# Kernel tuning notes

Measured on AMD Instinct MI355X. Metric: run time of the kernel, lower is better.

The kernel has to match this reference:

```python
import jax, jax.numpy as jnp
import numpy as np

B, L, D_IN, D_EDGE, H, D = 2, 384, 256, 128, 8, 32
SCALE = D ** (-0.5)


def setup_inputs() -> dict:
    key = jax.random.key(0)
    ks = jax.random.split(key, 12)
    hd = H * D
    s_in = D_IN ** -0.5
    s_e = D_EDGE ** -0.5
    return {
        "node_feat": jax.random.normal(ks[0], (B, L, D_IN), jnp.float32),
        "edge_feat": jax.random.normal(ks[1], (B, L, L, D_EDGE), jnp.float32),
        "edge_mask": (jax.random.uniform(ks[2], (B, L, L)) > 0.15).astype(jnp.float32),
        "Wq": jax.random.normal(ks[3], (D_IN, hd), jnp.float32) * s_in,
        "bq": jnp.zeros((hd,), jnp.float32),
        "Wk": jax.random.normal(ks[4], (D_IN, hd), jnp.float32) * s_in,
        "bk": jnp.zeros((hd,), jnp.float32),
        "Wv": jax.random.normal(ks[5], (D_IN, hd), jnp.float32) * s_in,
        "bv": jnp.zeros((hd,), jnp.float32),
        "We": jax.random.normal(ks[6], (D_EDGE, hd), jnp.float32) * s_e,
        "Wu": jax.random.normal(ks[7], (D_IN, hd), jnp.float32) * s_in,
        "bu": jnp.zeros((hd,), jnp.float32),
    }


def _split_heads(t):
    # (b, l, h*d) -> (b, h, l, d)
    b, l, _ = t.shape
    return t.reshape(b, l, H, D).transpose(0, 2, 1, 3)


def reference(node_feat, edge_feat, edge_mask, Wq, bq, Wk, bk, Wv, bv, We, Wu, bu):
    q = _split_heads(node_feat @ Wq + bq)
    k = _split_heads(node_feat @ Wk + bk)
    v = _split_heads(node_feat @ Wv + bv)
    # edge embedding: (b, i, j, h*d) -> (b, h, i, j, d)
    b, l = edge_feat.shape[0], edge_feat.shape[1]
    e = (edge_feat @ We).reshape(b, l, l, H, D).transpose(0, 3, 1, 2, 4)
    logit = jnp.einsum('bhid,bhjd->bhij', q, k)
    logit = logit + jnp.einsum('bhid,bhijd->bhij', q, e)
    att = logit * SCALE
    att = att + ((1.0 - edge_mask) * -1e9)[:, None, :, :]
    att = jax.nn.softmax(att, axis=-1)  # dropout is identity in eval / p=0
    updated = jnp.einsum('bhij,bhjd->bhid', att, v)
    updated = updated + jnp.einsum('bhij,bhijd->bhid', att, e)
    updated = updated.transpose(0, 2, 1, 3).reshape(b, l, H * D)
    return (node_feat @ Wu + bu) + updated
```

## Files before the change

kernel.cpp:

```cpp
#include <hip/hip_runtime.h>
#include <hip/hip_bf16.h>
#include <cstdint>

#define NB 2
#define LL 384
#define DIN 256
#define DE 128
#define NH 8
#define DH 32
#define HD 256
#define TJ 32
#define NTILES (LL / TJ)
#define SCALE 0.17677669529663687f

typedef __attribute__((ext_vector_type(8))) short bf16x8;
typedef __attribute__((ext_vector_type(4))) float f32x4;

static __device__ __forceinline__ unsigned short f2bf(float f) {
    uint32_t u = __builtin_bit_cast(uint32_t, f);
    u += 0x7FFF + ((u >> 16) & 1);
    return (unsigned short)(u >> 16);
}
static __device__ __forceinline__ float bf2f(unsigned short u) {
    return __builtin_bit_cast(float, (uint32_t)u << 16);
}
static __device__ __forceinline__ float getf4(const float4& v, int k) {
    return k == 0 ? v.x : k == 1 ? v.y : k == 2 ? v.z : v.w;
}

__global__ __launch_bounds__(128) void prep_we(const float* __restrict__ We,
                                               unsigned short* __restrict__ WeT) {
    const int n = blockIdx.x;
    const int k = threadIdx.x;
    WeT[n * DE + k] = f2bf(We[(size_t)k * HD + n]);
}

__global__ __launch_bounds__(256) void proj_kernel(
    const float* __restrict__ node,
    const float* __restrict__ Wq, const float* __restrict__ bq,
    const float* __restrict__ Wk, const float* __restrict__ bk,
    const float* __restrict__ Wv, const float* __restrict__ bv,
    const float* __restrict__ Wu, const float* __restrict__ bu,
    unsigned short* __restrict__ qb16, unsigned short* __restrict__ kb16,
    float* __restrict__ vb, float* __restrict__ ub)
{
    __shared__ __align__(16) float rows[4][DIN];
    const int t  = threadIdx.x;
    const int r0 = blockIdx.x * 4;

    #pragma unroll
    for (int r = 0; r < 4; ++r)
        rows[r][t] = node[(size_t)(r0 + r) * DIN + t];
    __syncthreads();

    float aq[4], ak[4], av[4], au[4];
    {
        const float vq = bq[t], vk = bk[t], vv = bv[t], vu = bu[t];
        #pragma unroll
        for (int r = 0; r < 4; ++r) { aq[r] = vq; ak[r] = vk; av[r] = vv; au[r] = vu; }
    }

    for (int f4 = 0; f4 < DIN / 4; ++f4) {
        float4 xv[4];
        #pragma unroll
        for (int r = 0; r < 4; ++r)
            xv[r] = *(const float4*)&rows[r][f4 * 4];
        #pragma unroll
        for (int k = 0; k < 4; ++k) {
            const int f = f4 * 4 + k;
            const float wq = Wq[(size_t)f * HD + t];
            const float wk = Wk[(size_t)f * HD + t];
            const float wv = Wv[(size_t)f * HD + t];
            const float wu = Wu[(size_t)f * HD + t];
            #pragma unroll
            for (int r = 0; r < 4; ++r) {
                const float x = getf4(xv[r], k);
                aq[r] += x * wq; ak[r] += x * wk; av[r] += x * wv; au[r] += x * wu;
            }
        }
    }

    #pragma unroll
    for (int r = 0; r < 4; ++r) {
        const size_t o = (size_t)(r0 + r) * HD + t;
        qb16[o] = f2bf(aq[r]); kb16[o] = f2bf(ak[r]);
        vb[o] = av[r]; ub[o] = au[r];
    }
}

__global__ __launch_bounds__(256) void vt_kernel(const float* __restrict__ vb,
                                                 unsigned short* __restrict__ vT) {
    __shared__ float tile[64][65];
    int blk = blockIdx.x;
    const int b  = blk / 24; blk %= 24;
    const int jt = blk / 4;
    const int ct = blk % 4;
    const int j0 = jt * 64, c0 = ct * 64;
    const int t  = threadIdx.x;
    const int c  = t & 63, j4 = t >> 6;
    #pragma unroll
    for (int rr = 0; rr < 16; ++rr) {
        const int j = j4 + 4 * rr;
        tile[j][c] = vb[(size_t)(b * LL + j0 + j) * HD + c0 + c];
    }
    __syncthreads();
    const int jj = t & 63, c4 = t >> 6;
    #pragma unroll
    for (int rr = 0; rr < 16; ++rr) {
        const int cc = c4 + 4 * rr;
        vT[(size_t)(b * HD + c0 + cc) * LL + j0 + jj] = f2bf(tile[jj][cc]);
    }
}

__global__ __launch_bounds__(256) void qk_kernel(
    const unsigned short* __restrict__ qb16, const unsigned short* __restrict__ kb16,
    const float* __restrict__ mask, float* __restrict__ logit_pre)
{
    int idx = blockIdx.x;
    const int jt = idx % 6; idx /= 6;
    const int it = idx % 6; idx /= 6;
    const int h  = idx % NH;
    const int b  = idx / NH;
    const int t    = threadIdx.x;
    const int lane = t & 63;
    const int w    = t >> 6;
    const int lid  = lane & 15;
    const int g    = lane >> 4;
    const int i0 = it * 64 + w * 16;
    const int j0 = jt * 64;

    const bf16x8 afr = *(const bf16x8*)&qb16[(size_t)(b * LL + i0 + lid) * HD + h * DH + g * 8];
    f32x4 acc[4];
    #pragma unroll
    for (int jj = 0; jj < 4; ++jj) {
        const bf16x8 bfrg = *(const bf16x8*)&kb16[(size_t)(b * LL + j0 + jj * 16 + lid) * HD + h * DH + g * 8];
        acc[jj] = __builtin_amdgcn_mfma_f32_16x16x32_bf16(afr, bfrg, (f32x4){0.f,0.f,0.f,0.f}, 0, 0, 0);
    }
    #pragma unroll
    for (int jj = 0; jj < 4; ++jj) {
        #pragma unroll
        for (int r = 0; r < 4; ++r) {
            const int i = i0 + 4 * g + r;
            const int j = j0 + jj * 16 + lid;
            const float lg = SCALE * acc[jj][r]
                           + (1.0f - mask[(size_t)(b * LL + i) * LL + j]) * -1e9f;
            logit_pre[((size_t)(b * NH + h) * LL + i) * LL + j] = lg;
        }
    }
}

__global__ __launch_bounds__(512, 4) void attn_kernel(
    const float* __restrict__ edge,
    const unsigned short* __restrict__ WeT,
    const float* __restrict__ logit_pre,
    const unsigned short* __restrict__ qb16,
    const unsigned short* __restrict__ vT,
    const float* __restrict__ ub,
    float* __restrict__ out)
{
    const int t    = threadIdx.x;
    const int lane = t & 63;
    const int w    = t >> 6;
    const int lid  = lane & 15;
    const int g    = lane >> 4;
    const int wb   = w * DH;
    const int bi   = blockIdx.x;
    const int b    = bi / LL;
    const int ii   = bi % LL;

    __shared__ __align__(16) unsigned short Es[2][TJ * DE];

    const float* efbase = edge + (size_t)bi * LL * DE;
    const float* lpre   = logit_pre + ((size_t)(b * NH + w) * LL + ii) * LL;
    const unsigned short* vTb = vT + (size_t)b * HD * LL;

    bf16x8 bfr[2][4];
    #pragma unroll
    for (int ct = 0; ct < 2; ++ct)
        #pragma unroll
        for (int kt = 0; kt < 4; ++kt)
            bfr[ct][kt] = *(const bf16x8*)&WeT[(size_t)(wb + ct * 16 + lid) * DE + kt * 32 + g * 8];

    float qf[2];
    #pragma unroll
    for (int ct = 0; ct < 2; ++ct)
        qf[ct] = bf2f(qb16[(size_t)bi * HD + wb + ct * 16 + lid]) * SCALE;

    const int sr = t >> 4;
    const int ci = t & 15;
    const int wchunk = (ci ^ (sr & 15)) << 3;

    const int jl_self = (((lid >> 2) & 1) << 4) + 4 * g + (lid & 3);

    float m_run = -3e38f, l_run = 0.0f;
    float out_p[2] = {0.f, 0.f};

    {
        const float* src = efbase + (size_t)sr * DE + ci * 8;
        const float4 x0 = ((const float4*)src)[0];
        const float4 x1 = ((const float4*)src)[1];
        bf16x8 p0;
        p0[0]=(short)f2bf(x0.x); p0[1]=(short)f2bf(x0.y); p0[2]=(short)f2bf(x0.z); p0[3]=(short)f2bf(x0.w);
        p0[4]=(short)f2bf(x1.x); p0[5]=(short)f2bf(x1.y); p0[6]=(short)f2bf(x1.z); p0[7]=(short)f2bf(x1.w);
        *(bf16x8*)&Es[0][sr * DE + wchunk] = p0;
    }

    for (int tile = 0; tile < NTILES; ++tile) {
        const int j0  = tile * TJ;
        const int cur = tile & 1;
        const unsigned short* Ecur = Es[cur];
        __syncthreads();

        const bool have_next = (tile + 1 < NTILES);
        float4 nx0, nx1;
        if (have_next) {
            const float* src = efbase + (size_t)(j0 + TJ + sr) * DE + ci * 8;
            nx0 = ((const float4*)src)[0];
            nx1 = ((const float4*)src)[1];
        }
        const float qkm = lpre[j0 + jl_self];
        ushort4 vld[2][2];
        #pragma unroll
        for (int ct = 0; ct < 2; ++ct)
            #pragma unroll
            for (int mm = 0; mm < 2; ++mm)
                vld[ct][mm] = *(const ushort4*)&vTb[(size_t)(wb + ct * 16 + lid) * LL + j0 + mm * 16 + 4 * g];

        f32x4 acc[2][2];
        #pragma unroll
        for (int mm = 0; mm < 2; ++mm)
            #pragma unroll
            for (int ct = 0; ct < 2; ++ct)
                acc[mm][ct] = (f32x4){0.f, 0.f, 0.f, 0.f};

        #pragma unroll
        for (int kt = 0; kt < 4; ++kt) {
            const int ch = kt * 4 + g;
            const bf16x8 a0 = *(const bf16x8*)&Ecur[lid * DE + ((ch ^ lid) << 3)];
            const bf16x8 a1 = *(const bf16x8*)&Ecur[(16 + lid) * DE + ((ch ^ lid) << 3)];
            #pragma unroll
            for (int ct = 0; ct < 2; ++ct) {
                acc[0][ct] = __builtin_amdgcn_mfma_f32_16x16x32_bf16(a0, bfr[ct][kt], acc[0][ct], 0, 0, 0);
                acc[1][ct] = __builtin_amdgcn_mfma_f32_16x16x32_bf16(a1, bfr[ct][kt], acc[1][ct], 0, 0, 0);
            }
        }

        float plog[8];
        #pragma unroll
        for (int mm = 0; mm < 2; ++mm)
            #pragma unroll
            for (int rg = 0; rg < 4; ++rg)
                plog[mm * 4 + rg] = acc[mm][0][rg] * qf[0] + acc[mm][1][rg] * qf[1];

        #pragma unroll
        for (int i2 = 0; i2 < 8; ++i2) plog[i2] += __shfl_xor(plog[i2], 8);
        float v4[4];
        {
            const bool hi = (lane & 4) != 0;
            #pragma unroll
            for (int r = 0; r < 4; ++r) {
                const float k2 = hi ? plog[4 + r] : plog[r];
                const float s2 = hi ? plog[r] : plog[4 + r];
                v4[r] = k2 + __shfl_xor(s2, 4);
            }
        }
        float v2[2];
        {
            const bool hi = (lane & 2) != 0;
            #pragma unroll
            for (int c2 = 0; c2 < 2; ++c2) {
                const float k2 = hi ? v4[2 + c2] : v4[c2];
                const float s2 = hi ? v4[c2] : v4[2 + c2];
                v2[c2] = k2 + __shfl_xor(s2, 2);
            }
        }
        float lgv;
        {
            const bool hi = (lane & 1) != 0;
            const float k2 = hi ? v2[1] : v2[0];
            const float s2 = hi ? v2[0] : v2[1];
            lgv = k2 + __shfl_xor(s2, 1);
        }
        const float lg = lgv + qkm;

        float mt = lg;
        #pragma unroll
        for (int off = 1; off < 64; off <<= 1) mt = fmaxf(mt, __shfl_xor(mt, off));
        const float mn = fmaxf(m_run, mt);
        const float p  = __expf(lg - mn);
        float ps = p;
        #pragma unroll
        for (int off = 1; off < 64; off <<= 1) ps += __shfl_xor(ps, off);
        const float fs = __expf(m_run - mn);
        l_run = l_run * fs + ps * 0.5f;
        m_run = mn;

        float pp[8];
        #pragma unroll
        for (int mm = 0; mm < 2; ++mm)
            #pragma unroll
            for (int rg = 0; rg < 4; ++rg)
                pp[mm * 4 + rg] = __shfl(p, (lane & 48) + mm * 4 + rg);

        out_p[0] *= fs; out_p[1] *= fs;
        #pragma unroll
        for (int ct = 0; ct < 2; ++ct)
            #pragma unroll
            for (int mm = 0; mm < 2; ++mm) {
                const ushort4 vv = vld[ct][mm];
                out_p[ct] += pp[mm * 4 + 0] * (bf2f(vv.x) + acc[mm][ct][0]);
                out_p[ct] += pp[mm * 4 + 1] * (bf2f(vv.y) + acc[mm][ct][1]);
                out_p[ct] += pp[mm * 4 + 2] * (bf2f(vv.z) + acc[mm][ct][2]);
                out_p[ct] += pp[mm * 4 + 3] * (bf2f(vv.w) + acc[mm][ct][3]);
            }

        if (have_next) {
            bf16x8 p0;
            p0[0]=(short)f2bf(nx0.x); p0[1]=(short)f2bf(nx0.y); p0[2]=(short)f2bf(nx0.z); p0[3]=(short)f2bf(nx0.w);
            p0[4]=(short)f2bf(nx1.x); p0[5]=(short)f2bf(nx1.y); p0[6]=(short)f2bf(nx1.z); p0[7]=(short)f2bf(nx1.w);
            *(bf16x8*)&Es[cur ^ 1][sr * DE + wchunk] = p0;
        }
    }

    #pragma unroll
    for (int ct = 0; ct < 2; ++ct) {
        out_p[ct] += __shfl_xor(out_p[ct], 16);
        out_p[ct] += __shfl_xor(out_p[ct], 32);
    }
    if (lane < 16) {
        const float inv = 1.0f / l_run;
        #pragma unroll
        for (int ct = 0; ct < 2; ++ct) {
            const int col = wb + ct * 16 + lane;
            out[(size_t)bi * HD + col] = ub[(size_t)bi * HD + col] + out_p[ct] * inv;
        }
    }
}

extern "C" void kernel_launch(void* const* d_in, const int* in_sizes, int n_in,
                              void* d_out, int out_size, void* d_ws, size_t ws_size,
                              hipStream_t stream) {
    const float* node = (const float*)d_in[0];
    const float* edge = (const float*)d_in[1];
    const float* mask = (const float*)d_in[2];
    const float* Wq   = (const float*)d_in[3];
    const float* bq   = (const float*)d_in[4];
    const float* Wk   = (const float*)d_in[5];
    const float* bk   = (const float*)d_in[6];
    const float* Wv   = (const float*)d_in[7];
    const float* bv   = (const float*)d_in[8];
    const float* We   = (const float*)d_in[9];
    const float* Wu   = (const float*)d_in[10];
    const float* bu   = (const float*)d_in[11];
    float* out = (float*)d_out;

    const size_t rowsz = (size_t)NB * LL * HD;
    float* ws   = (float*)d_ws;
    float* vb   = ws;
    float* ubuf = vb + rowsz;
    float* lpre = ubuf + rowsz;
    unsigned short* us   = (unsigned short*)(lpre + (size_t)NB * NH * LL * LL);
    unsigned short* WeT  = us;
    unsigned short* qb16 = WeT + (size_t)HD * DE;
    unsigned short* kb16 = qb16 + rowsz;
    unsigned short* vT   = kb16 + rowsz;

    hipLaunchKernelGGL(prep_we, dim3(HD), dim3(DE), 0, stream, We, WeT);
    hipLaunchKernelGGL(proj_kernel, dim3(NB * LL / 4), dim3(256), 0, stream,
                       node, Wq, bq, Wk, bk, Wv, bv, Wu, bu, qb16, kb16, vb, ubuf);
    hipLaunchKernelGGL(vt_kernel, dim3(NB * (LL / 64) * (HD / 64)), dim3(256), 0, stream,
                       vb, vT);
    hipLaunchKernelGGL(qk_kernel, dim3(NB * NH * (LL / 64) * (LL / 64)), dim3(256), 0, stream,
                       qb16, kb16, mask, lpre);
    hipLaunchKernelGGL(attn_kernel, dim3(NB * LL), dim3(512), 0, stream,
                       edge, WeT, lpre, qb16, vT, ubuf, out);
}
```

Baseline: 101.8 us.

## Reassociate edge projection: fold q into We and apply We after att·edge

Replaces the fused flash-style attention kernel with three kernels. The first precomputes q·We^T per node so edge logits come from edge·(qWe), a 128-wide product instead of projecting each edge to 256 dims. The second computes an exact two-pass softmax in place over the stored logits. The third computes att·edge and att·V with MFMA, then multiplies the aggregated edge sum by We afterwards. This cuts the edge GEMM FLOPs, but the edge tensor is now read from HBM twice and there are extra launches and a logit-buffer round trip.

New measurement: 118.7 us. 16.6% more time.

```diff
diff --git a/kernel.cpp b/kernel.cpp
--- a/kernel.cpp
+++ b/kernel.cpp
@@ -1,5 +1,4 @@
 #include <hip/hip_runtime.h>
-#include <hip/hip_bf16.h>
 #include <cstdint>
 
 #define NB 2
@@ -9,8 +8,6 @@
 #define NH 8
 #define DH 32
 #define HD 256
-#define TJ 32
-#define NTILES (LL / TJ)
 #define SCALE 0.17677669529663687f
 
 typedef __attribute__((ext_vector_type(8))) short bf16x8;
@@ -26,6 +23,12 @@
 }
 static __device__ __forceinline__ float getf4(const float4& v, int k) {
     return k == 0 ? v.x : k == 1 ? v.y : k == 2 ? v.z : v.w;
+}
+static __device__ __forceinline__ bf16x8 pack8(const float4& a, const float4& b) {
+    bf16x8 p;
+    p[0]=(short)f2bf(a.x); p[1]=(short)f2bf(a.y); p[2]=(short)f2bf(a.z); p[3]=(short)f2bf(a.w);
+    p[4]=(short)f2bf(b.x); p[5]=(short)f2bf(b.y); p[6]=(short)f2bf(b.z); p[7]=(short)f2bf(b.w);
+    return p;
 }
 
 __global__ __launch_bounds__(128) void prep_we(const float* __restrict__ We,
@@ -149,191 +152,216 @@
     }
 }
 
-__global__ __launch_bounds__(512, 4) void attn_kernel(
+__global__ __launch_bounds__(256) void qwe_kernel(
+    const unsigned short* __restrict__ qb16, const unsigned short* __restrict__ WeT,
+    unsigned short* __restrict__ qWe)
+{
+    const int bi = blockIdx.x;
+    const int t  = threadIdx.x;
+    const int h  = t >> 5;
+    const int c0 = (t & 31) * 4;
+
+    float qv[32];
+    const unsigned short* qp = &qb16[(size_t)bi * HD + h * DH];
+    #pragma unroll
+    for (int d = 0; d < 32; ++d) qv[d] = bf2f(qp[d]);
+
+    float acc0 = 0.f, acc1 = 0.f, acc2 = 0.f, acc3 = 0.f;
+    #pragma unroll
+    for (int d = 0; d < 32; ++d) {
+        const ushort4 wt = *(const ushort4*)&WeT[(size_t)(h * DH + d) * DE + c0];
+        acc0 += qv[d] * bf2f(wt.x); acc1 += qv[d] * bf2f(wt.y);
+        acc2 += qv[d] * bf2f(wt.z); acc3 += qv[d] * bf2f(wt.w);
+    }
+    unsigned short* o = &qWe[(size_t)bi * (NH * DE) + h * DE + c0];
+    o[0] = f2bf(SCALE * acc0); o[1] = f2bf(SCALE * acc1);
+    o[2] = f2bf(SCALE * acc2); o[3] = f2bf(SCALE * acc3);
+}
+
+__global__ __launch_bounds__(512, 4) void att_kernel(
     const float* __restrict__ edge,
+    const unsigned short* __restrict__ qWe,
+    float* __restrict__ lpre)
+{
+    __shared__ float red0[64], red1[64];
+    const int t = threadIdx.x, lane = t & 63, w = t >> 6;
+    const int lid = lane & 15, g = lane >> 4;
+    const int bi = blockIdx.x, b = bi / LL, ii = bi % LL;
+    const int J  = w * 48;
+    const int hq = lid & 7;
+
+    bf16x8 bfr[4];
+    const unsigned short* qwp = &qWe[(size_t)bi * (NH * DE) + hq * DE];
+    #pragma unroll
+    for (int kt = 0; kt < 4; ++kt)
+        bfr[kt] = *(const bf16x8*)&qwp[kt * 32 + g * 8];
+
+    f32x4 acc[3];
+    #pragma unroll
+    for (int mt = 0; mt < 3; ++mt) {
+        acc[mt] = (f32x4){0.f, 0.f, 0.f, 0.f};
+        const float* ef = edge + ((size_t)bi * LL + J + mt * 16 + lid) * DE;
+        #pragma unroll
+        for (int kt = 0; kt < 4; ++kt) {
+            const float4 x0 = *(const float4*)&ef[kt * 32 + g * 8];
+            const float4 x1 = *(const float4*)&ef[kt * 32 + g * 8 + 4];
+            acc[mt] = __builtin_amdgcn_mfma_f32_16x16x32_bf16(pack8(x0, x1), bfr[kt], acc[mt], 0, 0, 0);
+        }
+    }
+
+    float lg[12];
+    float* lrow = lpre + ((size_t)(b * NH + hq) * LL + ii) * LL;
+    #pragma unroll
+    for (int mt = 0; mt < 3; ++mt)
+        #pragma unroll
+        for (int r = 0; r < 4; ++r) {
+            const int j = J + mt * 16 + g * 4 + r;
+            lg[mt * 4 + r] = (lid < 8) ? (acc[mt][r] + lrow[j]) : -3e38f;
+        }
+
+    float m = lg[0];
+    #pragma unroll
+    for (int k = 1; k < 12; ++k) m = fmaxf(m, lg[k]);
+    m = fmaxf(m, __shfl_xor(m, 16));
+    m = fmaxf(m, __shfl_xor(m, 32));
+    if (lane < 8) red0[w * 8 + lane] = m;
+    __syncthreads();
+    float M = red0[hq];
+    #pragma unroll
+    for (int k = 1; k < 8; ++k) M = fmaxf(M, red0[k * 8 + hq]);
+
+    float p[12], s = 0.f;
+    #pragma unroll
+    for (int k = 0; k < 12; ++k) { p[k] = __expf(lg[k] - M); s += p[k]; }
+    s += __shfl_xor(s, 16); s += __shfl_xor(s, 32);
+    if (lane < 8) red1[w * 8 + lane] = s;
+    __syncthreads();
+    float S = 0.f;
+    #pragma unroll
+    for (int k = 0; k < 8; ++k) S += red1[k * 8 + hq];
+    const float inv = 1.0f / S;
+
+    if (lid < 8) {
+        #pragma unroll
+        for (int mt = 0; mt < 3; ++mt)
+            #pragma unroll
+            for (int r = 0; r < 4; ++r)
+                lrow[J + mt * 16 + g * 4 + r] = p[mt * 4 + r] * inv;
+    }
+}
+
+#define TJ 64
+#define NT (LL / TJ)
+__global__ __launch_bounds__(512, 4) void pv_kernel(
+    const float* __restrict__ edge,
+    const float* __restrict__ att,
+    const unsigned short* __restrict__ vT,
     const unsigned short* __restrict__ WeT,
-    const float* __restrict__ logit_pre,
-    const unsigned short* __restrict__ qb16,
-    const unsigned short* __restrict__ vT,
     const float* __restrict__ ub,
     float* __restrict__ out)
 {
-    const int t    = threadIdx.x;
-    const int lane = t & 63;
-    const int w    = t >> 6;
-    const int lid  = lane & 15;
-    const int g    = lane >> 4;
-    const int wb   = w * DH;
-    const int bi   = blockIdx.x;
-    const int b    = bi / LL;
-    const int ii   = bi % LL;
-
     __shared__ __align__(16) unsigned short Es[2][TJ * DE];
-
+    __shared__ __align__(16) unsigned short atts[NH * LL];
+    __shared__ float smA[NH * DE];
+    __shared__ float avs[HD];
+
+    const int t = threadIdx.x, lane = t & 63, w = t >> 6;
+    const int lid = lane & 15, g = lane >> 4;
+    const int bi = blockIdx.x, b = bi / LL, ii = bi % LL;
     const float* efbase = edge + (size_t)bi * LL * DE;
-    const float* lpre   = logit_pre + ((size_t)(b * NH + w) * LL + ii) * LL;
-    const unsigned short* vTb = vT + (size_t)b * HD * LL;
-
-    bf16x8 bfr[2][4];
-    #pragma unroll
-    for (int ct = 0; ct < 2; ++ct)
-        #pragma unroll
-        for (int kt = 0; kt < 4; ++kt)
-            bfr[ct][kt] = *(const bf16x8*)&WeT[(size_t)(wb + ct * 16 + lid) * DE + kt * 32 + g * 8];
-
-    float qf[2];
-    #pragma unroll
-    for (int ct = 0; ct < 2; ++ct)
-        qf[ct] = bf2f(qb16[(size_t)bi * HD + wb + ct * 16 + lid]) * SCALE;
-
-    const int sr = t >> 4;
-    const int ci = t & 15;
-    const int wchunk = (ci ^ (sr & 15)) << 3;
-
-    const int jl_self = (((lid >> 2) & 1) << 4) + 4 * g + (lid & 3);
-
-    float m_run = -3e38f, l_run = 0.0f;
-    float out_p[2] = {0.f, 0.f};
 
     {
+        const float* ar = att + ((size_t)(b * NH + w) * LL + ii) * LL;
+        #pragma unroll
+        for (int k = 0; k < 3; ++k) {
+            const int j2 = (lane + 64 * k) * 2;
+            const float2 x = *(const float2*)&ar[j2];
+            const unsigned int pk = ((unsigned int)f2bf(x.y) << 16) | (unsigned int)f2bf(x.x);
+            *(unsigned int*)&atts[w * LL + j2] = pk;
+        }
+    }
+    #pragma unroll
+    for (int q = 0; q < 2; ++q) {
+        const int id = t + q * 512, sr = id >> 4, ci = id & 15;
         const float* src = efbase + (size_t)sr * DE + ci * 8;
-        const float4 x0 = ((const float4*)src)[0];
-        const float4 x1 = ((const float4*)src)[1];
-        bf16x8 p0;
-        p0[0]=(short)f2bf(x0.x); p0[1]=(short)f2bf(x0.y); p0[2]=(short)f2bf(x0.z); p0[3]=(short)f2bf(x0.w);
-        p0[4]=(short)f2bf(x1.x); p0[5]=(short)f2bf(x1.y); p0[6]=(short)f2bf(x1.z); p0[7]=(short)f2bf(x1.w);
-        *(bf16x8*)&Es[0][sr * DE + wchunk] = p0;
-    }
-
-    for (int tile = 0; tile < NTILES; ++tile) {
+        const float4 x0 = ((const float4*)src)[0], x1 = ((const float4*)src)[1];
+        *(bf16x8*)&Es[0][sr * DE + ci * 8] = pack8(x0, x1);
+    }
+    __syncthreads();
+
+    f32x4 accE = (f32x4){0.f, 0.f, 0.f, 0.f};
+    f32x4 accV[2];
+    accV[0] = (f32x4){0.f, 0.f, 0.f, 0.f};
+    accV[1] = (f32x4){0.f, 0.f, 0.f, 0.f};
+
+    for (int tile = 0; tile < NT; ++tile) {
         const int j0  = tile * TJ;
         const int cur = tile & 1;
         const unsigned short* Ecur = Es[cur];
+        const bool have_next = (tile + 1 < NT);
+        float4 nx[2][2];
+        if (have_next) {
+            #pragma unroll
+            for (int q = 0; q < 2; ++q) {
+                const int id = t + q * 512, sr = id >> 4, ci = id & 15;
+                const float* src = efbase + (size_t)(j0 + TJ + sr) * DE + ci * 8;
+                nx[q][0] = ((const float4*)src)[0];
+                nx[q][1] = ((const float4*)src)[1];
+            }
+        }
+        #pragma unroll
+        for (int kt = 0; kt < 2; ++kt) {
+            const int jb = j0 + kt * 32;
+            const bf16x8 bf = *(const bf16x8*)&atts[(lid & 7) * LL + jb + g * 8];
+            bf16x8 ae;
+            #pragma unroll
+            for (int u = 0; u < 8; ++u)
+                ae[u] = (short)Ecur[(kt * 32 + g * 8 + u) * DE + 16 * w + lid];
+            accE = __builtin_amdgcn_mfma_f32_16x16x32_bf16(ae, bf, accE, 0, 0, 0);
+            #pragma unroll
+            for (int mt = 0; mt < 2; ++mt) {
+                const bf16x8 va = *(const bf16x8*)&vT[(size_t)(b * HD + w * DH + mt * 16 + lid) * LL + jb + g * 8];
+                accV[mt] = __builtin_amdgcn_mfma_f32_16x16x32_bf16(va, bf, accV[mt], 0, 0, 0);
+            }
+        }
+        if (have_next) {
+            #pragma unroll
+            for (int q = 0; q < 2; ++q) {
+                const int id = t + q * 512, sr = id >> 4, ci = id & 15;
+                *(bf16x8*)&Es[cur ^ 1][sr * DE + ci * 8] = pack8(nx[q][0], nx[q][1]);
+            }
+        }
         __syncthreads();
-
-        const bool have_next = (tile + 1 < NTILES);
-        float4 nx0, nx1;
-        if (have_next) {
-            const float* src = efbase + (size_t)(j0 + TJ + sr) * DE + ci * 8;
-            nx0 = ((const float4*)src)[0];
-            nx1 = ((const float4*)src)[1];
-        }
-        const float qkm = lpre[j0 + jl_self];
-        ushort4 vld[2][2];
-        #pragma unroll
-        for (int ct = 0; ct < 2; ++ct)
-            #pragma unroll
-            for (int mm = 0; mm < 2; ++mm)
-                vld[ct][mm] = *(const ushort4*)&vTb[(size_t)(wb + ct * 16 + lid) * LL + j0 + mm * 16 + 4 * g];
-
-        f32x4 acc[2][2];
-        #pragma unroll
-        for (int mm = 0; mm < 2; ++mm)
-            #pragma unroll
-            for (int ct = 0; ct < 2; ++ct)
-                acc[mm][ct] = (f32x4){0.f, 0.f, 0.f, 0.f};
-
-        #pragma unroll
-        for (int kt = 0; kt < 4; ++kt) {
-            const int ch = kt * 4 + g;
-            const bf16x8 a0 = *(const bf16x8*)&Ecur[lid * DE + ((ch ^ lid) << 3)];
-            const bf16x8 a1 = *(const bf16x8*)&Ecur[(16 + lid) * DE + ((ch ^ lid) << 3)];
-            #pragma unroll
-            for (int ct = 0; ct < 2; ++ct) {
-                acc[0][ct] = __builtin_amdgcn_mfma_f32_16x16x32_bf16(a0, bfr[ct][kt], acc[0][ct], 0, 0, 0);
-                acc[1][ct] = __builtin_amdgcn_mfma_f32_16x16x32_bf16(a1, bfr[ct][kt], acc[1][ct], 0, 0, 0);
-            }
-        }
-
-        float plog[8];
-        #pragma unroll
-        for (int mm = 0; mm < 2; ++mm)
-            #pragma unroll
-            for (int rg = 0; rg < 4; ++rg)
-                plog[mm * 4 + rg] = acc[mm][0][rg] * qf[0] + acc[mm][1][rg] * qf[1];
-
-        #pragma unroll
-        for (int i2 = 0; i2 < 8; ++i2) plog[i2] += __shfl_xor(plog[i2], 8);
-        float v4[4];
-        {
-            const bool hi = (lane & 4) != 0;
-            #pragma unroll
-            for (int r = 0; r < 4; ++r) {
-                const float k2 = hi ? plog[4 + r] : plog[r];
-                const float s2 = hi ? plog[r] : plog[4 + r];
-                v4[r] = k2 + __shfl_xor(s2, 4);
-            }
-        }
-        float v2[2];
-        {
-            const bool hi = (lane & 2) != 0;
-            #pragma unroll
-            for (int c2 = 0; c2 < 2; ++c2) {
-                const float k2 = hi ? v4[2 + c2] : v4[c2];
-                const float s2 = hi ? v4[c2] : v4[2 + c2];
-                v2[c2] = k2 + __shfl_xor(s2, 2);
-            }
-        }
-        float lgv;
-        {
-            const bool hi = (lane & 1) != 0;
-            const float k2 = hi ? v2[1] : v2[0];
-            const float s2 = hi ? v2[0] : v2[1];
-            lgv = k2 + __shfl_xor(s2, 1);
-        }
-        const float lg = lgv + qkm;
-
-        float mt = lg;
-        #pragma unroll
-        for (int off = 1; off < 64; off <<= 1) mt = fmaxf(mt, __shfl_xor(mt, off));
-        const float mn = fmaxf(m_run, mt);
-        const float p  = __expf(lg - mn);
-        float ps = p;
-        #pragma unroll
-        for (int off = 1; off < 64; off <<= 1) ps += __shfl_xor(ps, off);
-        const float fs = __expf(m_run - mn);
-        l_run = l_run * fs + ps * 0.5f;
-        m_run = mn;
-
-        float pp[8];
-        #pragma unroll
-        for (int mm = 0; mm < 2; ++mm)
-            #pragma unroll
-            for (int rg = 0; rg < 4; ++rg)
-                pp[mm * 4 + rg] = __shfl(p, (lane & 48) + mm * 4 + rg);
-
-        out_p[0] *= fs; out_p[1] *= fs;
-        #pragma unroll
-        for (int ct = 0; ct < 2; ++ct)
-            #pragma unroll
-            for (int mm = 0; mm < 2; ++mm) {
-                const ushort4 vv = vld[ct][mm];
-                out_p[ct] += pp[mm * 4 + 0] * (bf2f(vv.x) + acc[mm][ct][0]);
-                out_p[ct] += pp[mm * 4 + 1] * (bf2f(vv.y) + acc[mm][ct][1]);
-                out_p[ct] += pp[mm * 4 + 2] * (bf2f(vv.z) + acc[mm][ct][2]);
-                out_p[ct] += pp[mm * 4 + 3] * (bf2f(vv.w) + acc[mm][ct][3]);
-            }
-
-        if (have_next) {
-            bf16x8 p0;
-            p0[0]=(short)f2bf(nx0.x); p0[1]=(short)f2bf(nx0.y); p0[2]=(short)f2bf(nx0.z); p0[3]=(short)f2bf(nx0.w);
-            p0[4]=(short)f2bf(nx1.x); p0[5]=(short)f2bf(nx1.y); p0[6]=(short)f2bf(nx1.z); p0[7]=(short)f2bf(nx1.w);
-            *(bf16x8*)&Es[cur ^ 1][sr * DE + wchunk] = p0;
-        }
-    }
-
-    #pragma unroll
-    for (int ct = 0; ct < 2; ++ct) {
-        out_p[ct] += __shfl_xor(out_p[ct], 16);
-        out_p[ct] += __shfl_xor(out_p[ct], 32);
-    }
-    if (lane < 16) {
-        const float inv = 1.0f / l_run;
-        #pragma unroll
-        for (int ct = 0; ct < 2; ++ct) {
-            const int col = wb + ct * 16 + lane;
-            out[(size_t)bi * HD + col] = ub[(size_t)bi * HD + col] + out_p[ct] * inv;
-        }
+    }
+
+    if (lid < 8) {
+        #pragma unroll
+        for (int r = 0; r < 4; ++r)
+            smA[lid * DE + 16 * w + 4 * g + r] = accE[r];
+    }
+    if (lid == w) {
+        #pragma unroll
+        for (int mt = 0; mt < 2; ++mt)
+            #pragma unroll
+            for (int r = 0; r < 4; ++r)
+                avs[w * DH + mt * 16 + 4 * g + r] = accV[mt][r];
+    }
+    __syncthreads();
+
+    if (lane < 32) {
+        const int hd = w * DH + lane;
+        float o = ub[(size_t)bi * HD + hd] + avs[hd];
+        const unsigned short* wrow = &WeT[(size_t)hd * DE];
+        const float* sa = &smA[w * DE];
+        #pragma unroll
+        for (int c = 0; c < DE; c += 4) {
+            const ushort4 wt = *(const ushort4*)&wrow[c];
+            o += sa[c]     * bf2f(wt.x);
+            o += sa[c + 1] * bf2f(wt.y);
+            o += sa[c + 2] * bf2f(wt.z);
+            o += sa[c + 3] * bf2f(wt.w);
+        }
+        out[(size_t)bi * HD + hd] = o;
     }
 }
 
@@ -364,6 +392,7 @@
     unsigned short* qb16 = WeT + (size_t)HD * DE;
     unsigned short* kb16 = qb16 + rowsz;
     unsigned short* vT   = kb16 + rowsz;
+    unsigned short* qWeB = vT + rowsz;
 
     hipLaunchKernelGGL(prep_we, dim3(HD), dim3(DE), 0, stream, We, WeT);
     hipLaunchKernelGGL(proj_kernel, dim3(NB * LL / 4), dim3(256), 0, stream,
@@ -372,6 +401,10 @@
                        vb, vT);
     hipLaunchKernelGGL(qk_kernel, dim3(NB * NH * (LL / 64) * (LL / 64)), dim3(256), 0, stream,
                        qb16, kb16, mask, lpre);
-    hipLaunchKernelGGL(attn_kernel, dim3(NB * LL), dim3(512), 0, stream,
-                       edge, WeT, lpre, qb16, vT, ubuf, out);
-}
+    hipLaunchKernelGGL(qwe_kernel, dim3(NB * LL), dim3(256), 0, stream,
+                       qb16, WeT, qWeB);
+    hipLaunchKernelGGL(att_kernel, dim3(NB * LL), dim3(512), 0, stream,
+                       edge, qWeB, lpre);
+    hipLaunchKernelGGL(pv_kernel, dim3(NB * LL), dim3(512), 0, stream,
+                       edge, lpre, vT, WeT, ubuf, out);
+}
```

## Double the edge tile along j to 64 and raise MFMA wave priority

Applied to the files above, without the earlier changes.

Doubles the number of j rows processed per tile, from 32 to 64. Each wave now issues four MFMA row blocks per k-step, the butterfly reduction gains an extra stage, and each thread stages two edge rows per prefetch. This halves the number of tiles, barriers and softmax reductions per row. The previous 0.5 factor on the probability sum is removed because each lane now holds a unique logit. s_setprio is raised around the MFMA loop. The cost is more registers (acc, plog, vld) and twice the LDS per buffer, which may lower occupancy.

After: 131.7 us. 29.4% more time.

```diff
diff --git a/kernel.cpp b/kernel.cpp
--- a/kernel.cpp
+++ b/kernel.cpp
@@ -9,7 +9,7 @@
 #define NH 8
 #define DH 32
 #define HD 256
-#define TJ 32
+#define TJ 64
 #define NTILES (LL / TJ)
 #define SCALE 0.17677669529663687f
 
@@ -26,6 +26,12 @@
 }
 static __device__ __forceinline__ float getf4(const float4& v, int k) {
     return k == 0 ? v.x : k == 1 ? v.y : k == 2 ? v.z : v.w;
+}
+static __device__ __forceinline__ bf16x8 pack8(const float4& a, const float4& b) {
+    bf16x8 p;
+    p[0]=(short)f2bf(a.x); p[1]=(short)f2bf(a.y); p[2]=(short)f2bf(a.z); p[3]=(short)f2bf(a.w);
+    p[4]=(short)f2bf(b.x); p[5]=(short)f2bf(b.y); p[6]=(short)f2bf(b.z); p[7]=(short)f2bf(b.w);
+    return p;
 }
 
 __global__ __launch_bounds__(128) void prep_we(const float* __restrict__ We,
@@ -190,19 +196,18 @@
     const int ci = t & 15;
     const int wchunk = (ci ^ (sr & 15)) << 3;
 
-    const int jl_self = (((lid >> 2) & 1) << 4) + 4 * g + (lid & 3);
+    const int jl_self = ((lid >> 2) & 3) * 16 + 4 * g + (lid & 3);
 
     float m_run = -3e38f, l_run = 0.0f;
     float out_p[2] = {0.f, 0.f};
 
-    {
-        const float* src = efbase + (size_t)sr * DE + ci * 8;
+    #pragma unroll
+    for (int q = 0; q < 2; ++q) {
+        const int row = sr + 32 * q;
+        const float* src = efbase + (size_t)row * DE + ci * 8;
         const float4 x0 = ((const float4*)src)[0];
         const float4 x1 = ((const float4*)src)[1];
-        bf16x8 p0;
-        p0[0]=(short)f2bf(x0.x); p0[1]=(short)f2bf(x0.y); p0[2]=(short)f2bf(x0.z); p0[3]=(short)f2bf(x0.w);
-        p0[4]=(short)f2bf(x1.x); p0[5]=(short)f2bf(x1.y); p0[6]=(short)f2bf(x1.z); p0[7]=(short)f2bf(x1.w);
-        *(bf16x8*)&Es[0][sr * DE + wchunk] = p0;
+        *(bf16x8*)&Es[0][row * DE + wchunk] = pack8(x0, x1);
     }
 
     for (int tile = 0; tile < NTILES; ++tile) {
@@ -212,56 +217,71 @@
         __syncthreads();
 
         const bool have_next = (tile + 1 < NTILES);
-        float4 nx0, nx1;
+        float4 nx[2][2];
         if (have_next) {
-            const float* src = efbase + (size_t)(j0 + TJ + sr) * DE + ci * 8;
-            nx0 = ((const float4*)src)[0];
-            nx1 = ((const float4*)src)[1];
+            #pragma unroll
+            for (int q = 0; q < 2; ++q) {
+                const float* src = efbase + (size_t)(j0 + TJ + sr + 32 * q) * DE + ci * 8;
+                nx[q][0] = ((const float4*)src)[0];
+                nx[q][1] = ((const float4*)src)[1];
+            }
         }
         const float qkm = lpre[j0 + jl_self];
-        ushort4 vld[2][2];
+        ushort4 vld[2][4];
         #pragma unroll
         for (int ct = 0; ct < 2; ++ct)
             #pragma unroll
-            for (int mm = 0; mm < 2; ++mm)
+            for (int mm = 0; mm < 4; ++mm)
                 vld[ct][mm] = *(const ushort4*)&vTb[(size_t)(wb + ct * 16 + lid) * LL + j0 + mm * 16 + 4 * g];
 
-        f32x4 acc[2][2];
-        #pragma unroll
-        for (int mm = 0; mm < 2; ++mm)
+        f32x4 acc[4][2];
+        #pragma unroll
+        for (int mm = 0; mm < 4; ++mm)
             #pragma unroll
             for (int ct = 0; ct < 2; ++ct)
                 acc[mm][ct] = (f32x4){0.f, 0.f, 0.f, 0.f};
 
+        __builtin_amdgcn_s_setprio(1);
         #pragma unroll
         for (int kt = 0; kt < 4; ++kt) {
             const int ch = kt * 4 + g;
-            const bf16x8 a0 = *(const bf16x8*)&Ecur[lid * DE + ((ch ^ lid) << 3)];
-            const bf16x8 a1 = *(const bf16x8*)&Ecur[(16 + lid) * DE + ((ch ^ lid) << 3)];
-            #pragma unroll
-            for (int ct = 0; ct < 2; ++ct) {
-                acc[0][ct] = __builtin_amdgcn_mfma_f32_16x16x32_bf16(a0, bfr[ct][kt], acc[0][ct], 0, 0, 0);
-                acc[1][ct] = __builtin_amdgcn_mfma_f32_16x16x32_bf16(a1, bfr[ct][kt], acc[1][ct], 0, 0, 0);
-            }
-        }
-
-        float plog[8];
-        #pragma unroll
-        for (int mm = 0; mm < 2; ++mm)
+            bf16x8 a[4];
+            #pragma unroll
+            for (int mm = 0; mm < 4; ++mm)
+                a[mm] = *(const bf16x8*)&Ecur[(mm * 16 + lid) * DE + ((ch ^ lid) << 3)];
+            #pragma unroll
+            for (int ct = 0; ct < 2; ++ct)
+                #pragma unroll
+                for (int mm = 0; mm < 4; ++mm)
+                    acc[mm][ct] = __builtin_amdgcn_mfma_f32_16x16x32_bf16(a[mm], bfr[ct][kt], acc[mm][ct], 0, 0, 0);
+        }
+        __builtin_amdgcn_s_setprio(0);
+
+        float plog[16];
+        #pragma unroll
+        for (int mm = 0; mm < 4; ++mm)
             #pragma unroll
             for (int rg = 0; rg < 4; ++rg)
                 plog[mm * 4 + rg] = acc[mm][0][rg] * qf[0] + acc[mm][1][rg] * qf[1];
 
-        #pragma unroll
-        for (int i2 = 0; i2 < 8; ++i2) plog[i2] += __shfl_xor(plog[i2], 8);
+        float v8[8];
+        {
+            const bool hi = (lane & 8) != 0;
+            #pragma unroll
+            for (int k = 0; k < 8; ++k) {
+                const float keep = hi ? plog[8 + k] : plog[k];
+                const float send = hi ? plog[k] : plog[8 + k];
+                v8[k] = keep + __shfl_xor(send, 8);
+            }
+        }
         float v4[4];
         {
             const bool hi = (lane & 4) != 0;
             #pragma unroll
             for (int r = 0; r < 4; ++r) {
-                const float k2 = hi ? plog[4 + r] : plog[r];
-                const float s2 = hi ? plog[r] : plog[4 + r];
-                v4[r] = k2 + __shfl_xor(s2, 4);
+                const float keep = hi ? v8[4 + r] : v8[r];
+                const float send = hi ? v8[r] : v8[4 + r];
+                v4[r] = keep + __shfl_xor(send, 4);
             }
         }
         float v2[2];
@@ -269,17 +289,17 @@
             const bool hi = (lane & 2) != 0;
             #pragma unroll
             for (int c2 = 0; c2 < 2; ++c2) {
-                const float k2 = hi ? v4[2 + c2] : v4[c2];
-                const float s2 = hi ? v4[c2] : v4[2 + c2];
-                v2[c2] = k2 + __shfl_xor(s2, 2);
+                const float keep = hi ? v4[2 + c2] : v4[c2];
+                const float send = hi ? v4[c2] : v4[2 + c2];
+                v2[c2] = keep + __shfl_xor(send, 2);
             }
         }
         float lgv;
         {
             const bool hi = (lane & 1) != 0;
-            const float k2 = hi ? v2[1] : v2[0];
-            const float s2 = hi ? v2[0] : v2[1];
-            lgv = k2 + __shfl_xor(s2, 1);
+            const float keep = hi ? v2[1] : v2[0];
+            const float send = hi ? v2[0] : v2[1];
+            lgv = keep + __shfl_xor(send, 1);
         }
         const float lg = lgv + qkm;
 
@@ -292,12 +312,12 @@
         #pragma unroll
         for (int off = 1; off < 64; off <<= 1) ps += __shfl_xor(ps, off);
         const float fs = __expf(m_run - mn);
-        l_run = l_run * fs + ps * 0.5f;
+        l_run = l_run * fs + ps;
         m_run = mn;
 
-        float pp[8];
-        #pragma unroll
-        for (int mm = 0; mm < 2; ++mm)
+        float pp[16];
+        #pragma unroll
+        for (int mm = 0; mm < 4; ++mm)
             #pragma unroll
             for (int rg = 0; rg < 4; ++rg)
                 pp[mm * 4 + rg] = __shfl(p, (lane & 48) + mm * 4 + rg);
@@ -306,7 +326,7 @@
         #pragma unroll
         for (int ct = 0; ct < 2; ++ct)
             #pragma unroll
-            for (int mm = 0; mm < 2; ++mm) {
+            for (int mm = 0; mm < 4; ++mm) {
                 const ushort4 vv = vld[ct][mm];
                 out_p[ct] += pp[mm * 4 + 0] * (bf2f(vv.x) + acc[mm][ct][0]);
                 out_p[ct] += pp[mm * 4 + 1] * (bf2f(vv.y) + acc[mm][ct][1]);
@@ -315,10 +335,9 @@
             }
 
         if (have_next) {
-            bf16x8 p0;
-            p0[0]=(short)f2bf(nx0.x); p0[1]=(short)f2bf(nx0.y); p0[2]=(short)f2bf(nx0.z); p0[3]=(short)f2bf(nx0.w);
-            p0[4]=(short)f2bf(nx1.x); p0[5]=(short)f2bf(nx1.y); p0[6]=(short)f2bf(nx1.z); p0[7]=(short)f2bf(nx1.w);
-            *(bf16x8*)&Es[cur ^ 1][sr * DE + wchunk] = p0;
+            #pragma unroll
+            for (int q = 0; q < 2; ++q)
+                *(bf16x8*)&Es[cur ^ 1][(sr + 32 * q) * DE + wchunk] = pack8(nx[q][0], nx[q][1]);
         }
     }
 
```
